# Kernel optimization log

Measured on AMD Instinct MI355X. Metric: run time of the kernel, lower is better.

Reference implementation:

```python
import jax, jax.numpy as jnp
import numpy as np

B, S, DIN, DOUT = 2, 2048, 4096, 4096


def setup_inputs() -> dict:
    key = jax.random.key(0)
    k1, k2 = jax.random.split(key)
    x = jax.random.normal(k1, (B, S, DIN), dtype=jnp.float32)
    weight = jax.random.normal(k2, (DOUT, DIN), dtype=jnp.float32) * 0.02
    # xnor init for row scaling pattern
    mean = weight.mean(-1, keepdims=True)                      # [DOUT,1]
    scale = jnp.abs(weight - mean).mean(-1, keepdims=True)     # [DOUT,1]
    wscale = scale
    wbias = mean
    return {"x": x, "weight": weight, "wscale": wscale, "wbias": wbias}


def reference(x, weight, wscale, wbias):
    # STE binarization: forward = sign(weight) (grad handled in bwd module)
    w_bin = jnp.sign(weight)
    w = wscale * w_bin + wbias                                 # [DOUT, DIN]
    # F.linear(x, w): x @ w.T, no bias
    out = jnp.einsum('bsk,nk->bsn', x, w)
    return out
```

## Files before the change

### kernel.cpp

```cpp
#include <hip/hip_runtime.h>
#include <stdint.h>


#define MDIM 4096
#define NDIM 4096
#define KDIM 4096

typedef int int4v __attribute__((ext_vector_type(4)));

__device__ __forceinline__ int pack4_rn(float a, float b, float c, float d, float inv) {
  int ia = __float2int_rn(a * inv) & 0xff;
  int ib = __float2int_rn(b * inv) & 0xff;
  int ic = __float2int_rn(c * inv) & 0xff;
  int id = __float2int_rn(d * inv) & 0xff;
  return ia | (ib << 8) | (ic << 16) | (id << 24);
}

__device__ __forceinline__ int sgn8(float v) {
  return (v > 0.f) ? 1 : ((v < 0.f) ? 0xff : 0);
}

__global__ __launch_bounds__(256) void prep_kernel(
    const float* __restrict__ x, const float* __restrict__ w,
    char* __restrict__ xq, char* __restrict__ wsg,
    float* __restrict__ xscale, float* __restrict__ sumx) {
  const int b = blockIdx.x;
  const int tid = threadIdx.x;
  if (b < MDIM) {
    const int row = b;
    const float4* xr = (const float4*)(x + (size_t)row * KDIM);
    float4 v[4];
    float s = 0.f, amax = 0.f;
#pragma unroll
    for (int u = 0; u < 4; ++u) {
      v[u] = xr[u * 256 + tid];
      s += v[u].x + v[u].y + v[u].z + v[u].w;
      amax = fmaxf(amax, fmaxf(fmaxf(fabsf(v[u].x), fabsf(v[u].y)),
                               fmaxf(fabsf(v[u].z), fabsf(v[u].w))));
    }
#pragma unroll
    for (int off = 32; off > 0; off >>= 1) {
      s += __shfl_down(s, off, 64);
      amax = fmaxf(amax, __shfl_down(amax, off, 64));
    }
    __shared__ float rs[4], rm[4], bcast;
    if ((tid & 63) == 0) { rs[tid >> 6] = s; rm[tid >> 6] = amax; }
    __syncthreads();
    if (tid == 0) {
      sumx[row] = rs[0] + rs[1] + rs[2] + rs[3];
      float mt = fmaxf(fmaxf(rm[0], rm[1]), fmaxf(rm[2], rm[3]));
      xscale[row] = mt * (1.f / 127.f);
      bcast = (mt > 0.f) ? 127.f / mt : 0.f;
    }
    __syncthreads();
    const float inv = bcast;
    int* xo = (int*)(xq + (size_t)row * KDIM);
#pragma unroll
    for (int u = 0; u < 4; ++u)
      xo[u * 256 + tid] = pack4_rn(v[u].x, v[u].y, v[u].z, v[u].w, inv);
  } else {
    const size_t base = (size_t)(b - MDIM) * (256 * 4);
    const float4* wr = (const float4*)w;
    int* wo = (int*)wsg;
#pragma unroll
    for (int u = 0; u < 4; ++u) {
      size_t i = base + u * 256 + tid;
      float4 v = wr[i];
      wo[i] = sgn8(v.x) | (sgn8(v.y) << 8) | (sgn8(v.z) << 16) | (sgn8(v.w) << 24);
    }
  }
}

__global__ __launch_bounds__(512, 2) void gemm_bin_i8_8phase(
    const char* __restrict__ A, const char* __restrict__ Bs,
    const float* __restrict__ wscale, const float* __restrict__ wbias,
    const float* __restrict__ xscale, const float* __restrict__ sumx,
    float* __restrict__ C) {
  __shared__ __align__(16) char sm[131072];

  const int bm = blockIdx.x >> 4, bn = blockIdx.x & 15;
  const int tm0 = bm * 256, tn0 = bn * 256;
  const int tid = threadIdx.x;
  const int lane = tid & 63, wave = tid >> 6;
  const int quad = lane >> 4, l16 = lane & 15;
  const int wr = wave >> 2, wc = wave & 3;

  int4v acc[2][4][4];
  const int4v zero4 = {0, 0, 0, 0};
#pragma unroll
  for (int rh = 0; rh < 2; ++rh)
#pragma unroll
    for (int i = 0; i < 4; ++i)
#pragma unroll
      for (int j = 0; j < 4; ++j) acc[rh][i][j] = zero4;

  int4v bf[4];

  int aOff[2][4];
#pragma unroll
  for (int rh = 0; rh < 2; ++rh)
#pragma unroll
    for (int i = 0; i < 4; ++i) {
      int row = wr * 128 + rh * 64 + i * 16 + l16;
      int sw = (row ^ (row >> 2)) & 3;
      aOff[rh][i] = row * 64 + ((quad ^ sw) & 3) * 16;
    }
  int bOff[4];
#pragma unroll
  for (int j = 0; j < 4; ++j) {
    int row = wc * 64 + j * 16 + l16;
    int sw = (row ^ (row >> 2)) & 3;
    bOff[j] = 65536 + row * 64 + ((quad ^ sw) & 3) * 16;
  }

  const int u0 = tid, u1 = tid + 512;
  const int r0 = u0 >> 2, r1 = u1 >> 2;
  const int c0 = (u0 & 3) ^ ((r0 ^ (r0 >> 2)) & 3);
  const int c1 = (u1 & 3) ^ ((r1 ^ (r1 >> 2)) & 3);
  const char* gA0 = A + (size_t)(tm0 + r0) * KDIM + c0 * 16;
  const char* gA1 = A + (size_t)(tm0 + r1) * KDIM + c1 * 16;
  const char* gB0 = Bs + (size_t)(tn0 + r0) * KDIM + c0 * 16;
  const char* gB1 = Bs + (size_t)(tn0 + r1) * KDIM + c1 * 16;
  const int ldsu0 = tid * 16, ldsu1 = 8192 + tid * 16;

#define STAGE_A(BUF, KH, KOFS)                                                    \
  do {                                                                            \
    const int base_ = ((BUF) * 2 + (KH)) * 16384;                                 \
    __builtin_amdgcn_global_load_lds(                                             \
        (const __attribute__((address_space(1))) void*)(gA0 + (KOFS)),            \
        (__attribute__((address_space(3))) void*)(sm + base_ + ldsu0), 16, 0, 0); \
    __builtin_amdgcn_global_load_lds(                                             \
        (const __attribute__((address_space(1))) void*)(gA1 + (KOFS)),            \
        (__attribute__((address_space(3))) void*)(sm + base_ + ldsu1), 16, 0, 0); \
  } while (0)

#define STAGE_B(BUF, KH, KOFS)                                                    \
  do {                                                                            \
    const int base_ = 65536 + ((BUF) * 2 + (KH)) * 16384;                         \
    __builtin_amdgcn_global_load_lds(                                             \
        (const __attribute__((address_space(1))) void*)(gB0 + (KOFS)),            \
        (__attribute__((address_space(3))) void*)(sm + base_ + ldsu0), 16, 0, 0); \
    __builtin_amdgcn_global_load_lds(                                             \
        (const __attribute__((address_space(1))) void*)(gB1 + (KOFS)),            \
        (__attribute__((address_space(3))) void*)(sm + base_ + ldsu1), 16, 0, 0); \
  } while (0)

#define BAR __builtin_amdgcn_s_barrier()
#define CK4 asm volatile("s_waitcnt vmcnt(4)\n\ts_barrier" ::: "memory")
#define CK0 asm volatile("s_waitcnt vmcnt(0)\n\ts_barrier" ::: "memory")

#define PHASE(BUF, KS, RH, CKBAR, ...)                                            \
  do {                                                                            \
    int4v af[4];                                                                  \
    _Pragma("unroll") for (int i_ = 0; i_ < 4; ++i_)                              \
        af[i_] = *(const int4v*)(sm + ((BUF) * 2 + (KS)) * 16384 + aOff[RH][i_]); \
    if ((RH) == 0) {                                                              \
      _Pragma("unroll") for (int j_ = 0; j_ < 4; ++j_)                            \
          bf[j_] = *(const int4v*)(sm + ((BUF) * 2 + (KS)) * 16384 + bOff[j_]);   \
    }                                                                             \
    __VA_ARGS__;                                                                  \
    __builtin_amdgcn_s_barrier();                                                 \
    asm volatile("s_waitcnt lgkmcnt(0)" ::: "memory");                            \
    __builtin_amdgcn_sched_barrier(0);                                            \
    __builtin_amdgcn_s_setprio(1);                                                \
    _Pragma("unroll") for (int i_ = 0; i_ < 4; ++i_)                              \
        _Pragma("unroll") for (int j_ = 0; j_ < 4; ++j_)                          \
            acc[RH][i_][j_] = __builtin_amdgcn_mfma_i32_16x16x64_i8(              \
                af[i_], bf[j_], acc[RH][i_][j_], 0, 0, 0);                        \
    __builtin_amdgcn_s_setprio(0);                                                \
    CKBAR;                                                                        \
  } while (0)

#define ITER_FULL(BUF, TAU)                                                       \
  do {                                                                            \
    PHASE(BUF, 0, 0, BAR, STAGE_A((BUF) ^ 1, 1, ((TAU) + 1) * 128 + 64));         \
    PHASE(BUF, 0, 1, BAR, STAGE_B((BUF) ^ 1, 1, ((TAU) + 1) * 128 + 64));         \
    PHASE(BUF, 1, 0, BAR, STAGE_A(BUF, 0, ((TAU) + 2) * 128));                    \
    PHASE(BUF, 1, 1, CK4, STAGE_B(BUF, 0, ((TAU) + 2) * 128));                    \
  } while (0)

  STAGE_A(0, 0, 0);
  STAGE_B(0, 0, 0);
  STAGE_A(0, 1, 64);
  STAGE_B(0, 1, 64);
  STAGE_A(1, 0, 128);
  STAGE_B(1, 0, 128);
  CK4;

#pragma unroll 1
  for (int t = 0; t < 30; t += 2) {
    ITER_FULL(0, t);
    ITER_FULL(1, t + 1);
  }
  PHASE(0, 0, 0, BAR, STAGE_A(1, 1, 31 * 128 + 64));
  PHASE(0, 0, 1, BAR, STAGE_B(1, 1, 31 * 128 + 64));
  PHASE(0, 1, 0, BAR, (void)0);
  PHASE(0, 1, 1, CK0, (void)0);
  PHASE(1, 0, 0, BAR, (void)0);
  PHASE(1, 0, 1, BAR, (void)0);
  PHASE(1, 1, 0, BAR, (void)0);
  PHASE(1, 1, 1, BAR, (void)0);

#undef ITER_FULL
#undef PHASE
#undef BAR
#undef CK4
#undef CK0
#undef STAGE_A
#undef STAGE_B

  float wsv[4], wbv[4];
#pragma unroll
  for (int j = 0; j < 4; ++j) {
    int n = tn0 + wc * 64 + j * 16 + l16;
    wsv[j] = wscale[n];
    wbv[j] = wbias[n];
  }
#pragma unroll
  for (int rh = 0; rh < 2; ++rh) {
#pragma unroll
    for (int i = 0; i < 4; ++i) {
#pragma unroll
      for (int r = 0; r < 4; ++r) {
        int m = tm0 + wr * 128 + rh * 64 + i * 16 + quad * 4 + r;
        float xs = xscale[m];
        float sx = sumx[m];
        float* crow = C + (size_t)m * NDIM + tn0 + wc * 64 + l16;
#pragma unroll
        for (int j = 0; j < 4; ++j)
          crow[j * 16] = wsv[j] * xs * (float)acc[rh][i][j][r] + wbv[j] * sx;
      }
    }
  }
}

extern "C" void kernel_launch(void* const* d_in, const int* in_sizes, int n_in,
                              void* d_out, int out_size, void* d_ws, size_t ws_size,
                              hipStream_t stream) {
  const float* x      = (const float*)d_in[0];
  const float* weight = (const float*)d_in[1];
  const float* wscale = (const float*)d_in[2];
  const float* wbias  = (const float*)d_in[3];
  float* out = (float*)d_out;

  char* xq  = (char*)d_ws;
  char* wsg = xq + (size_t)MDIM * KDIM;
  float* xscale = (float*)(wsg + (size_t)NDIM * KDIM);
  float* sumx   = xscale + MDIM;

  prep_kernel<<<MDIM + (NDIM * KDIM) / (16 * 256), 256, 0, stream>>>(
      x, weight, xq, wsg, xscale, sumx);
  gemm_bin_i8_8phase<<<(MDIM / 256) * (NDIM / 256), 512, 0, stream>>>(
      xq, wsg, wscale, wbias, xscale, sumx, out);
}
```

Before: 234.7 us.

## Switch int8 GEMM to 32x32x32 MFMA tiles with new LDS swizzle

Replaces the 16x16x64 int8 MFMA with the 32x32x32 variant. Each wave now holds a 4x2 grid of 32x32 accumulators, and each phase covers a 32-wide K slice instead of splitting the work into row halves. The LDS swizzle, fragment offsets and epilogue mapping are all rewritten to match. The goal is fewer MFMA issues and fewer fragment loads per tile, and the larger instruction may give higher throughput. In exchange it changes the LDS bank-conflict pattern and leaves the epilogue writes less coalesced.

```diff
diff --git a/kernel.cpp b/kernel.cpp
--- a/kernel.cpp
+++ b/kernel.cpp
@@ -6,7 +6,8 @@
 #define NDIM 4096
 #define KDIM 4096
 
-typedef int int4v __attribute__((ext_vector_type(4)));
+typedef int int4v  __attribute__((ext_vector_type(4)));
+typedef int int16v __attribute__((ext_vector_type(16)));
 
 __device__ __forceinline__ int pack4_rn(float a, float b, float c, float d, float inv) {
   int ia = __float2int_rn(a * inv) & 0xff;
@@ -82,41 +83,38 @@
   const int tm0 = bm * 256, tn0 = bn * 256;
   const int tid = threadIdx.x;
   const int lane = tid & 63, wave = tid >> 6;
-  const int quad = lane >> 4, l16 = lane & 15;
+  const int col32 = lane & 31, hl = lane >> 5;
   const int wr = wave >> 2, wc = wave & 3;
 
-  int4v acc[2][4][4];
-  const int4v zero4 = {0, 0, 0, 0};
-#pragma unroll
-  for (int rh = 0; rh < 2; ++rh)
-#pragma unroll
-    for (int i = 0; i < 4; ++i)
-#pragma unroll
-      for (int j = 0; j < 4; ++j) acc[rh][i][j] = zero4;
-
-  int4v bf[4];
-
-  int aOff[2][4];
-#pragma unroll
-  for (int rh = 0; rh < 2; ++rh)
-#pragma unroll
-    for (int i = 0; i < 4; ++i) {
-      int row = wr * 128 + rh * 64 + i * 16 + l16;
-      int sw = (row ^ (row >> 2)) & 3;
-      aOff[rh][i] = row * 64 + ((quad ^ sw) & 3) * 16;
-    }
-  int bOff[4];
-#pragma unroll
-  for (int j = 0; j < 4; ++j) {
-    int row = wc * 64 + j * 16 + l16;
-    int sw = (row ^ (row >> 2)) & 3;
-    bOff[j] = 65536 + row * 64 + ((quad ^ sw) & 3) * 16;
+  int16v acc[4][2];
+#pragma unroll
+  for (int mi = 0; mi < 4; ++mi)
+#pragma unroll
+    for (int nj = 0; nj < 2; ++nj)
+#pragma unroll
+      for (int r = 0; r < 16; ++r) acc[mi][nj][r] = 0;
+
+  int aOff[2][4], bOff[2][2];
+#pragma unroll
+  for (int ks2 = 0; ks2 < 2; ++ks2) {
+#pragma unroll
+    for (int mi = 0; mi < 4; ++mi) {
+      int row = wr * 128 + mi * 32 + col32;
+      int sw = (row >> 1) & 3;
+      aOff[ks2][mi] = row * 64 + (((ks2 * 2 + hl) ^ sw) & 3) * 16;
+    }
+#pragma unroll
+    for (int nj = 0; nj < 2; ++nj) {
+      int row = wc * 64 + nj * 32 + col32;
+      int sw = (row >> 1) & 3;
+      bOff[ks2][nj] = 65536 + row * 64 + (((ks2 * 2 + hl) ^ sw) & 3) * 16;
+    }
   }
 
   const int u0 = tid, u1 = tid + 512;
   const int r0 = u0 >> 2, r1 = u1 >> 2;
-  const int c0 = (u0 & 3) ^ ((r0 ^ (r0 >> 2)) & 3);
-  const int c1 = (u1 & 3) ^ ((r1 ^ (r1 >> 2)) & 3);
+  const int c0 = (u0 & 3) ^ ((r0 >> 1) & 3);
+  const int c1 = (u1 & 3) ^ ((r1 >> 1) & 3);
   const char* gA0 = A + (size_t)(tm0 + r0) * KDIM + c0 * 16;
   const char* gA1 = A + (size_t)(tm0 + r1) * KDIM + c1 * 16;
   const char* gB0 = Bs + (size_t)(tn0 + r0) * KDIM + c0 * 16;
@@ -149,24 +147,22 @@
 #define CK4 asm volatile("s_waitcnt vmcnt(4)\n\ts_barrier" ::: "memory")
 #define CK0 asm volatile("s_waitcnt vmcnt(0)\n\ts_barrier" ::: "memory")
 
-#define PHASE(BUF, KS, RH, CKBAR, ...)                                            \
-  do {                                                                            \
-    int4v af[4];                                                                  \
-    _Pragma("unroll") for (int i_ = 0; i_ < 4; ++i_)                              \
-        af[i_] = *(const int4v*)(sm + ((BUF) * 2 + (KS)) * 16384 + aOff[RH][i_]); \
-    if ((RH) == 0) {                                                              \
-      _Pragma("unroll") for (int j_ = 0; j_ < 4; ++j_)                            \
-          bf[j_] = *(const int4v*)(sm + ((BUF) * 2 + (KS)) * 16384 + bOff[j_]);   \
-    }                                                                             \
+#define PHASE(BUF, KS, KS2, CKBAR, ...)                                           \
+  do {                                                                            \
+    int4v af[4], bq[2];                                                           \
+    _Pragma("unroll") for (int mi_ = 0; mi_ < 4; ++mi_)                           \
+        af[mi_] = *(const int4v*)(sm + ((BUF) * 2 + (KS)) * 16384 + aOff[KS2][mi_]); \
+    _Pragma("unroll") for (int nj_ = 0; nj_ < 2; ++nj_)                           \
+        bq[nj_] = *(const int4v*)(sm + ((BUF) * 2 + (KS)) * 16384 + bOff[KS2][nj_]); \
     __VA_ARGS__;                                                                  \
     __builtin_amdgcn_s_barrier();                                                 \
     asm volatile("s_waitcnt lgkmcnt(0)" ::: "memory");                            \
     __builtin_amdgcn_sched_barrier(0);                                            \
     __builtin_amdgcn_s_setprio(1);                                                \
-    _Pragma("unroll") for (int i_ = 0; i_ < 4; ++i_)                              \
-        _Pragma("unroll") for (int j_ = 0; j_ < 4; ++j_)                          \
-            acc[RH][i_][j_] = __builtin_amdgcn_mfma_i32_16x16x64_i8(              \
-                af[i_], bf[j_], acc[RH][i_][j_], 0, 0, 0);                        \
+    _Pragma("unroll") for (int mi_ = 0; mi_ < 4; ++mi_)                           \
+        _Pragma("unroll") for (int nj_ = 0; nj_ < 2; ++nj_)                       \
+            acc[mi_][nj_] = __builtin_amdgcn_mfma_i32_32x32x32_i8(                \
+                af[mi_], bq[nj_], acc[mi_][nj_], 0, 0, 0);                        \
     __builtin_amdgcn_s_setprio(0);                                                \
     CKBAR;                                                                        \
   } while (0)
@@ -209,27 +205,24 @@
 #undef STAGE_A
 #undef STAGE_B
 
-  float wsv[4], wbv[4];
-#pragma unroll
-  for (int j = 0; j < 4; ++j) {
-    int n = tn0 + wc * 64 + j * 16 + l16;
-    wsv[j] = wscale[n];
-    wbv[j] = wbias[n];
-  }
-#pragma unroll
-  for (int rh = 0; rh < 2; ++rh) {
-#pragma unroll
-    for (int i = 0; i < 4; ++i) {
-#pragma unroll
-      for (int r = 0; r < 4; ++r) {
-        int m = tm0 + wr * 128 + rh * 64 + i * 16 + quad * 4 + r;
-        float xs = xscale[m];
-        float sx = sumx[m];
-        float* crow = C + (size_t)m * NDIM + tn0 + wc * 64 + l16;
-#pragma unroll
-        for (int j = 0; j < 4; ++j)
-          crow[j * 16] = wsv[j] * xs * (float)acc[rh][i][j][r] + wbv[j] * sx;
-      }
+  float wsv[2], wbv[2];
+#pragma unroll
+  for (int nj = 0; nj < 2; ++nj) {
+    int n = tn0 + wc * 64 + nj * 32 + col32;
+    wsv[nj] = wscale[n];
+    wbv[nj] = wbias[n];
+  }
+#pragma unroll
+  for (int mi = 0; mi < 4; ++mi) {
+#pragma unroll
+    for (int reg = 0; reg < 16; ++reg) {
+      int m = tm0 + wr * 128 + mi * 32 + (reg & 3) + 8 * (reg >> 2) + 4 * hl;
+      float xs = xscale[m];
+      float sx = sumx[m];
+      float* crow = C + (size_t)m * NDIM + tn0 + wc * 64 + col32;
+#pragma unroll
+      for (int nj = 0; nj < 2; ++nj)
+        crow[nj * 32] = wsv[nj] * xs * (float)acc[mi][nj][reg] + wbv[nj] * sx;
     }
   }
 }
```

Measured after the change: 236.7 us. No clear change (+0.9%).
